# Kernel optimization log

Hardware: AMD Instinct MI355X
Metric: run time of the kernel (lower is better)

Reference implementation:

```python
import jax, jax.numpy as jnp
import numpy as np

B, N, M = 262144, 8, 4  # batch, state_dim, meas_dim
EPS = 1e-6


def _psd(key, b, d, scale=1.0):
    A = jax.random.normal(key, (b, d, d), dtype=jnp.float32)
    return (A @ jnp.swapaxes(A, 1, 2)) / d * scale + 0.1 * jnp.eye(d, dtype=jnp.float32)


def setup_inputs() -> dict:
    key = jax.random.key(0)
    ks = jax.random.split(key, 7)
    x_est = jax.random.normal(ks[0], (B, N, 1), dtype=jnp.float32)
    P_est = _psd(ks[1], B, N)
    F = jnp.eye(N, dtype=jnp.float32) + 0.1 * jax.random.normal(ks[2], (B, N, N), dtype=jnp.float32)
    Q = _psd(ks[3], B, N, scale=0.1)
    z = jax.random.normal(ks[4], (B, M, 1), dtype=jnp.float32)
    H = jax.random.normal(ks[5], (B, M, N), dtype=jnp.float32)
    R = _psd(ks[6], B, M, scale=0.5)
    return {"x_est": x_est, "P_est": P_est, "F": F, "Q": Q, "z": z, "H": H, "R": R}


def reference(x_est, P_est, F, Q, z, H, R):
    # Predict: x_pred = F x, P_pred = F P F^T + Q
    x_pred = F @ x_est                                     # [B,n,1]
    P_pred = F @ P_est @ jnp.swapaxes(F, 1, 2) + Q         # [B,n,n]
    # Update
    H_T = jnp.swapaxes(H, 1, 2)                            # [B,n,m]
    S = H @ P_pred @ H_T + R + EPS * jnp.eye(M, dtype=P_pred.dtype)  # [B,m,m]
    S_inv = jnp.linalg.inv(S)
    K = P_pred @ H_T @ S_inv                               # [B,n,m]
    y = z - H @ x_pred                                     # innovation [B,m,1]
    x_new = x_pred + K @ y
    IKH = jnp.eye(N, dtype=P_pred.dtype) - K @ H           # [B,n,n]
    P_new = IKH @ P_pred
    return x_new, P_new, K
```

## Files before the change

kernel.cpp:

```cpp
#include <hip/hip_runtime.h>


#define EPS 1e-6f
#define SYMIDX(r, c) ((r) * ((r) + 1) / 2 + (c))

typedef float v4f __attribute__((ext_vector_type(4)));

__device__ __forceinline__ void wave_lds_fence() {
    asm volatile("s_waitcnt lgkmcnt(0)" ::: "memory");
    __builtin_amdgcn_wave_barrier();
}

template <int W>
__device__ __forceinline__ void stage_load(float4 (&tmp)[W / 4], const float* __restrict__ src,
                                           int lane, int maxchunk) {
    const float4* s4 = reinterpret_cast<const float4*>(src);
#pragma unroll
    for (int i = 0; i < W / 4; ++i) {
        int c = i * 64 + lane;
        if (c >= maxchunk) c = maxchunk - 1;
        tmp[i] = s4[c];
    }
}

template <int W>
__device__ __forceinline__ void stage_write(const float4 (&tmp)[W / 4], float* buf, int lane) {
    constexpr int STR = W + 4;
#pragma unroll
    for (int i = 0; i < W / 4; ++i) {
        int c = i * 64 + lane;
        int bb = c / (W / 4);
        int e = c & (W / 4 - 1);
        *reinterpret_cast<float4*>(buf + bb * STR + e * 4) = tmp[i];
    }
}

__global__ __launch_bounds__(64) __attribute__((amdgpu_waves_per_eu(2, 4)))
void kf_kernel(const float* __restrict__ x_est,
               const float* __restrict__ P_est,
               const float* __restrict__ Fin,
               const float* __restrict__ Qin,
               const float* __restrict__ zin,
               const float* __restrict__ Hin,
               const float* __restrict__ Rin,
               float* __restrict__ out, int B) {
    const int lane = threadIdx.x;
    const int blockBase = blockIdx.x * 64;
    const int nb = (B - blockBase < 64) ? (B - blockBase) : 64;
    const int b = blockBase + lane;
    const size_t sb = (size_t)((b < B) ? b : (B - 1));
    const size_t wbase = (size_t)blockBase;

    __shared__ __align__(16) float buf[64 * 68];

    float4 zz = reinterpret_cast<const float4*>(zin)[sb];
    float4 xa = reinterpret_cast<const float4*>(x_est)[2 * sb];
    float4 xb = reinterpret_cast<const float4*>(x_est)[2 * sb + 1];

    float4 tF[16];
    stage_load<64>(tF, Fin + wbase * 64, lane, nb * 16);
    stage_write<64>(tF, buf, lane);

    float4 tP[16];
    stage_load<64>(tP, P_est + wbase * 64, lane, nb * 16);

    wave_lds_fence();
    float Fr[64];
    {
        const float* my = buf + lane * 68;
#pragma unroll
        for (int r = 0; r < 8; ++r) {
            float4 a = *reinterpret_cast<const float4*>(my + r * 8);
            float4 c4 = *reinterpret_cast<const float4*>(my + r * 8 + 4);
            Fr[r * 8 + 0] = a.x;  Fr[r * 8 + 1] = a.y;  Fr[r * 8 + 2] = a.z;  Fr[r * 8 + 3] = a.w;
            Fr[r * 8 + 4] = c4.x; Fr[r * 8 + 5] = c4.y; Fr[r * 8 + 6] = c4.z; Fr[r * 8 + 7] = c4.w;
        }
    }

    float xp[8];
    {
        float x[8] = {xa.x, xa.y, xa.z, xa.w, xb.x, xb.y, xb.z, xb.w};
#pragma unroll
        for (int i = 0; i < 8; ++i) {
            float s = 0.f;
#pragma unroll
            for (int j = 0; j < 8; ++j) s += Fr[i * 8 + j] * x[j];
            xp[i] = s;
        }
    }

    wave_lds_fence();
    stage_write<64>(tP, buf, lane);

    float4 tQ[16];
    stage_load<64>(tQ, Qin + wbase * 64, lane, nb * 16);

    wave_lds_fence();
    float Ps[36];
    {
        const float* my = buf + lane * 68;
#pragma unroll
        for (int r = 0; r < 8; ++r) {
            float4 a = *reinterpret_cast<const float4*>(my + r * 8);
            float row[8];
            row[0] = a.x; row[1] = a.y; row[2] = a.z; row[3] = a.w;
            row[4] = row[5] = row[6] = row[7] = 0.f;
            if (r >= 4) {
                float4 c4 = *reinterpret_cast<const float4*>(my + r * 8 + 4);
                row[4] = c4.x; row[5] = c4.y; row[6] = c4.z; row[7] = c4.w;
            }
#pragma unroll
            for (int j = 0; j <= r; ++j) Ps[SYMIDX(r, j)] = row[j];
        }
    }

    wave_lds_fence();
    stage_write<64>(tQ, buf, lane);

    float4 tH[8];
    stage_load<32>(tH, Hin + wbase * 32, lane, nb * 8);

    wave_lds_fence();
    float Pps[36];
    {
        const float* myq = buf + lane * 68;
#pragma unroll
        for (int i = 0; i < 8; ++i) {
            float Ti[8];
#pragma unroll
            for (int j = 0; j < 8; ++j) {
                float s = 0.f;
#pragma unroll
                for (int k = 0; k < 8; ++k) {
                    float pkj = (k >= j) ? Ps[SYMIDX(k, j)] : Ps[SYMIDX(j, k)];
                    s += Fr[i * 8 + k] * pkj;
                }
                Ti[j] = s;
            }
            float4 qa = *reinterpret_cast<const float4*>(myq + i * 8);
            float4 qb = qa;
            if (i >= 4) qb = *reinterpret_cast<const float4*>(myq + i * 8 + 4);
            float Qr[8] = {qa.x, qa.y, qa.z, qa.w, qb.x, qb.y, qb.z, qb.w};
#pragma unroll
            for (int j = 0; j <= i; ++j) {
                float s = Qr[j];
#pragma unroll
                for (int k = 0; k < 8; ++k) s += Ti[k] * Fr[j * 8 + k];
                Pps[SYMIDX(i, j)] = s;
            }
        }
    }

    wave_lds_fence();
    stage_write<32>(tH, buf, lane);

    float4 tR[4];
    stage_load<16>(tR, Rin + wbase * 16, lane, nb * 4);

    wave_lds_fence();
    float Hm[32];
    {
        const float* my = buf + lane * 36;
#pragma unroll
        for (int r = 0; r < 4; ++r) {
            float4 a = *reinterpret_cast<const float4*>(my + r * 8);
            float4 c4 = *reinterpret_cast<const float4*>(my + r * 8 + 4);
            Hm[r * 8 + 0] = a.x;  Hm[r * 8 + 1] = a.y;  Hm[r * 8 + 2] = a.z;  Hm[r * 8 + 3] = a.w;
            Hm[r * 8 + 4] = c4.x; Hm[r * 8 + 5] = c4.y; Hm[r * 8 + 6] = c4.z; Hm[r * 8 + 7] = c4.w;
        }
    }

    wave_lds_fence();
    stage_write<16>(tR, buf, lane);

    float HP[32];
#pragma unroll
    for (int i = 0; i < 4; ++i)
#pragma unroll
        for (int j = 0; j < 8; ++j) {
            float s = 0.f;
#pragma unroll
            for (int k = 0; k < 8; ++k) {
                float pkj = (k >= j) ? Pps[SYMIDX(k, j)] : Pps[SYMIDX(j, k)];
                s += Hm[i * 8 + k] * pkj;
            }
            HP[i * 8 + j] = s;
        }

    float y[4];
    {
        float zv[4] = {zz.x, zz.y, zz.z, zz.w};
#pragma unroll
        for (int i = 0; i < 4; ++i) {
            float s = zv[i];
#pragma unroll
            for (int k = 0; k < 8; ++k) s -= Hm[i * 8 + k] * xp[k];
            y[i] = s;
        }
    }

    wave_lds_fence();
    float S[16];
    {
        const float* my = buf + lane * 20;
#pragma unroll
        for (int i = 0; i < 4; ++i) {
            float4 r4 = *reinterpret_cast<const float4*>(my + i * 4);
            float Rr[4] = {r4.x, r4.y, r4.z, r4.w};
#pragma unroll
            for (int j = 0; j < 4; ++j) {
                float s = Rr[j];
#pragma unroll
                for (int k = 0; k < 8; ++k) s += HP[i * 8 + k] * Hm[j * 8 + k];
                if (i == j) s += EPS;
                S[i * 4 + j] = s;
            }
        }
    }

    float inv[16];
    inv[0]  =  S[5]*S[10]*S[15] - S[5]*S[11]*S[14] - S[9]*S[6]*S[15] + S[9]*S[7]*S[14] + S[13]*S[6]*S[11] - S[13]*S[7]*S[10];
    inv[4]  = -S[4]*S[10]*S[15] + S[4]*S[11]*S[14] + S[8]*S[6]*S[15] - S[8]*S[7]*S[14] - S[12]*S[6]*S[11] + S[12]*S[7]*S[10];
    inv[8]  =  S[4]*S[9]*S[15]  - S[4]*S[11]*S[13] - S[8]*S[5]*S[15] + S[8]*S[7]*S[13] + S[12]*S[5]*S[11] - S[12]*S[7]*S[9];
    inv[12] = -S[4]*S[9]*S[14]  + S[4]*S[10]*S[13] + S[8]*S[5]*S[14] - S[8]*S[6]*S[13] - S[12]*S[5]*S[10] + S[12]*S[6]*S[9];
    inv[1]  = -S[1]*S[10]*S[15] + S[1]*S[11]*S[14] + S[9]*S[2]*S[15] - S[9]*S[3]*S[14] - S[13]*S[2]*S[11] + S[13]*S[3]*S[10];
    inv[5]  =  S[0]*S[10]*S[15] - S[0]*S[11]*S[14] - S[8]*S[2]*S[15] + S[8]*S[3]*S[14] + S[12]*S[2]*S[11] - S[12]*S[3]*S[10];
    inv[9]  = -S[0]*S[9]*S[15]  + S[0]*S[11]*S[13] + S[8]*S[1]*S[15] - S[8]*S[3]*S[13] - S[12]*S[1]*S[11] + S[12]*S[3]*S[9];
    inv[13] =  S[0]*S[9]*S[14]  - S[0]*S[10]*S[13] - S[8]*S[1]*S[14] + S[8]*S[2]*S[13] + S[12]*S[1]*S[10] - S[12]*S[2]*S[9];
    inv[2]  =  S[1]*S[6]*S[15]  - S[1]*S[7]*S[14]  - S[5]*S[2]*S[15] + S[5]*S[3]*S[14] + S[13]*S[2]*S[7]  - S[13]*S[3]*S[6];
    inv[6]  = -S[0]*S[6]*S[15]  + S[0]*S[7]*S[14]  + S[4]*S[2]*S[15] - S[4]*S[3]*S[14] - S[12]*S[2]*S[7]  + S[12]*S[3]*S[6];
    inv[10] =  S[0]*S[5]*S[15]  - S[0]*S[7]*S[13]  - S[4]*S[1]*S[15] + S[4]*S[3]*S[13] + S[12]*S[1]*S[7]  - S[12]*S[3]*S[5];
    inv[14] = -S[0]*S[5]*S[14]  + S[0]*S[6]*S[13]  + S[4]*S[1]*S[14] - S[4]*S[2]*S[13] - S[12]*S[1]*S[6]  + S[12]*S[2]*S[5];
    inv[3]  = -S[1]*S[6]*S[11]  + S[1]*S[7]*S[10]  + S[5]*S[2]*S[11] - S[5]*S[3]*S[10] - S[9]*S[2]*S[7]   + S[9]*S[3]*S[6];
    inv[7]  =  S[0]*S[6]*S[11]  - S[0]*S[7]*S[10]  - S[4]*S[2]*S[11] + S[4]*S[3]*S[10] + S[8]*S[2]*S[7]   - S[8]*S[3]*S[6];
    inv[11] = -S[0]*S[5]*S[11]  + S[0]*S[7]*S[9]   + S[4]*S[1]*S[11] - S[4]*S[3]*S[9]  - S[8]*S[1]*S[7]   + S[8]*S[3]*S[5];
    inv[15] =  S[0]*S[5]*S[10]  - S[0]*S[6]*S[9]   - S[4]*S[1]*S[10] + S[4]*S[2]*S[9]  + S[8]*S[1]*S[6]   - S[8]*S[2]*S[5];
    float det = S[0]*inv[0] + S[1]*inv[4] + S[2]*inv[8] + S[3]*inv[12];
    float rdet = 1.0f / det;
#pragma unroll
    for (int i = 0; i < 16; ++i) inv[i] *= rdet;

    float K[32];
#pragma unroll
    for (int i = 0; i < 8; ++i)
#pragma unroll
        for (int j = 0; j < 4; ++j) {
            float s = 0.f;
#pragma unroll
            for (int k = 0; k < 4; ++k) s += HP[k * 8 + i] * inv[k * 4 + j];
            K[i * 4 + j] = s;
        }

    if (b < B) {
        float xn[8];
#pragma unroll
        for (int i = 0; i < 8; ++i) {
            float s = xp[i];
#pragma unroll
            for (int k = 0; k < 4; ++k) s += K[i * 4 + k] * y[k];
            xn[i] = s;
        }
        v4f v0 = {xn[0], xn[1], xn[2], xn[3]};
        v4f v1 = {xn[4], xn[5], xn[6], xn[7]};
        v4f* xo = reinterpret_cast<v4f*>(out + (size_t)b * 8);
        __builtin_nontemporal_store(v0, xo);
        __builtin_nontemporal_store(v1, xo + 1);
    }

    wave_lds_fence();
    {
        float* my = buf + lane * 68;
#pragma unroll
        for (int i = 0; i < 8; ++i) {
            float r[8];
#pragma unroll
            for (int j = 0; j < 8; ++j) {
                float pij = (i >= j) ? Pps[SYMIDX(i, j)] : Pps[SYMIDX(j, i)];
                float s = pij;
#pragma unroll
                for (int k = 0; k < 4; ++k) s -= K[i * 4 + k] * HP[k * 8 + j];
                r[j] = s;
            }
            *reinterpret_cast<float4*>(my + i * 8)     = make_float4(r[0], r[1], r[2], r[3]);
            *reinterpret_cast<float4*>(my + i * 8 + 4) = make_float4(r[4], r[5], r[6], r[7]);
        }
    }
    wave_lds_fence();
    {
        float* outP = out + (size_t)B * 8 + wbase * 64;
        const int maxc = nb * 16;
#pragma unroll
        for (int i = 0; i < 16; ++i) {
            int c = i * 64 + lane;
            if (c < maxc) {
                int bb = c >> 4, e = c & 15;
                v4f v = *reinterpret_cast<const v4f*>(buf + bb * 68 + e * 4);
                __builtin_nontemporal_store(v, reinterpret_cast<v4f*>(outP) + c);
            }
        }
    }

    wave_lds_fence();
    {
        float* my = buf + lane * 36;
#pragma unroll
        for (int i = 0; i < 8; ++i)
            *reinterpret_cast<float4*>(my + i * 4) =
                make_float4(K[4 * i + 0], K[4 * i + 1], K[4 * i + 2], K[4 * i + 3]);
    }
    wave_lds_fence();
    {
        float* outK = out + (size_t)B * 72 + wbase * 32;
        const int maxc = nb * 8;
#pragma unroll
        for (int i = 0; i < 8; ++i) {
            int c = i * 64 + lane;
            if (c < maxc) {
                int bb = c >> 3, e = c & 7;
                v4f v = *reinterpret_cast<const v4f*>(buf + bb * 36 + e * 4);
                __builtin_nontemporal_store(v, reinterpret_cast<v4f*>(outK) + c);
            }
        }
    }
}

extern "C" void kernel_launch(void* const* d_in, const int* in_sizes, int n_in,
                              void* d_out, int out_size, void* d_ws, size_t ws_size,
                              hipStream_t stream) {
    const float* x_est = (const float*)d_in[0];
    const float* P_est = (const float*)d_in[1];
    const float* F     = (const float*)d_in[2];
    const float* Q     = (const float*)d_in[3];
    const float* z     = (const float*)d_in[4];
    const float* H     = (const float*)d_in[5];
    const float* R     = (const float*)d_in[6];
    float* out = (float*)d_out;
    int B = in_sizes[0] / 8;
    int block = 64;
    int grid = (B + 63) / 64;
    kf_kernel<<<grid, block, 0, stream>>>(x_est, P_est, F, Q, z, H, R, out, B);
}
```

Baseline: 358.8 us.

## Persistent grid with async global-to-LDS prefetch of next group's F/P/Q

Converts the kernel to a persistent grid-stride loop over 64-batch groups, capped at 768 blocks. While the current group is computed, the next group's F, P and Q are prefetched straight into XOR-swizzled LDS using global_load_lds. H and R are now read per-thread directly from global memory. Outputs are written with plain per-thread strided stores instead of staging through LDS for coalescing. A hand-tuned vmcnt wait and the lower occupancy hint risk stalls, uncoalesced store traffic, or correctness issues if the counter count is wrong.

```diff
diff --git a/kernel.cpp b/kernel.cpp
--- a/kernel.cpp
+++ b/kernel.cpp
@@ -4,38 +4,27 @@
 #define EPS 1e-6f
 #define SYMIDX(r, c) ((r) * ((r) + 1) / 2 + (c))
 
-typedef float v4f __attribute__((ext_vector_type(4)));
-
-__device__ __forceinline__ void wave_lds_fence() {
-    asm volatile("s_waitcnt lgkmcnt(0)" ::: "memory");
-    __builtin_amdgcn_wave_barrier();
+__device__ __forceinline__ void gl_lds16(const float* g, float* l) {
+    __builtin_amdgcn_global_load_lds(
+        (const __attribute__((address_space(1))) void*)(uintptr_t)g,
+        (__attribute__((address_space(3))) void*)(unsigned)(uintptr_t)l,
+        16, 0, 0);
 }
 
-template <int W>
-__device__ __forceinline__ void stage_load(float4 (&tmp)[W / 4], const float* __restrict__ src,
-                                           int lane, int maxchunk) {
-    const float4* s4 = reinterpret_cast<const float4*>(src);
-#pragma unroll
-    for (int i = 0; i < W / 4; ++i) {
-        int c = i * 64 + lane;
-        if (c >= maxchunk) c = maxchunk - 1;
-        tmp[i] = s4[c];
+__device__ __forceinline__ void stage64(const float* __restrict__ src, int gstart,
+                                        float* ldsbase, int lane, int B) {
+#pragma unroll
+    for (int i = 0; i < 16; ++i) {
+        int b = i * 4 + (lane >> 4);
+        int e = lane & 15;
+        int gb = gstart + b;
+        if (gb > B - 1) gb = B - 1;
+        gl_lds16(src + (size_t)gb * 64 + (size_t)((e ^ (b & 7)) * 4),
+                 ldsbase + i * 256);
     }
 }
 
-template <int W>
-__device__ __forceinline__ void stage_write(const float4 (&tmp)[W / 4], float* buf, int lane) {
-    constexpr int STR = W + 4;
-#pragma unroll
-    for (int i = 0; i < W / 4; ++i) {
-        int c = i * 64 + lane;
-        int bb = c / (W / 4);
-        int e = c & (W / 4 - 1);
-        *reinterpret_cast<float4*>(buf + bb * STR + e * 4) = tmp[i];
-    }
-}
-
-__global__ __launch_bounds__(64) __attribute__((amdgpu_waves_per_eu(2, 4)))
+__global__ __launch_bounds__(64) __attribute__((amdgpu_waves_per_eu(1)))
 void kf_kernel(const float* __restrict__ x_est,
                const float* __restrict__ P_est,
                const float* __restrict__ Fin,
@@ -45,85 +34,115 @@
                const float* __restrict__ Rin,
                float* __restrict__ out, int B) {
     const int lane = threadIdx.x;
-    const int blockBase = blockIdx.x * 64;
-    const int nb = (B - blockBase < 64) ? (B - blockBase) : 64;
-    const int b = blockBase + lane;
-    const size_t sb = (size_t)((b < B) ? b : (B - 1));
-    const size_t wbase = (size_t)blockBase;
-
-    __shared__ __align__(16) float buf[64 * 68];
-
-    float4 zz = reinterpret_cast<const float4*>(zin)[sb];
-    float4 xa = reinterpret_cast<const float4*>(x_est)[2 * sb];
-    float4 xb = reinterpret_cast<const float4*>(x_est)[2 * sb + 1];
-
-    float4 tF[16];
-    stage_load<64>(tF, Fin + wbase * 64, lane, nb * 16);
-    stage_write<64>(tF, buf, lane);
-
-    float4 tP[16];
-    stage_load<64>(tP, P_est + wbase * 64, lane, nb * 16);
-
-    wave_lds_fence();
-    float Fr[64];
-    {
-        const float* my = buf + lane * 68;
+    const int ngroups = (B + 63) >> 6;
+    int g = blockIdx.x;
+    if (g >= ngroups) return;
+    const int stride = gridDim.x;
+
+    __shared__ __align__(16) float lds[12288];
+
+    stage64(Fin, g * 64, lds, lane, B);
+    stage64(P_est, g * 64, lds + 4096, lane, B);
+    stage64(Qin, g * 64, lds + 8192, lane, B);
+    int bc = g * 64 + lane;
+    if (bc > B - 1) bc = B - 1;
+    float4 zz = reinterpret_cast<const float4*>(zin)[bc];
+    float4 xa = reinterpret_cast<const float4*>(x_est)[2 * bc];
+    float4 xb = reinterpret_cast<const float4*>(x_est)[2 * bc + 1];
+    asm volatile("s_waitcnt vmcnt(0)" ::: "memory");
+
+    while (true) {
+        const int b0 = g * 64 + lane;
+        const bool full = (g * 64 + 64 <= B);
+        const int sw = lane & 7;
+        const float4* L4 = reinterpret_cast<const float4*>(lds);
+        const int gn = g + stride;
+        const int gnc = (gn < ngroups) ? gn : 0;
+
+        int b0c = (b0 > B - 1) ? B - 1 : b0;
+        float Hm[32];
+        {
+            const float4* H4 = reinterpret_cast<const float4*>(Hin + (size_t)b0c * 32);
+#pragma unroll
+            for (int i = 0; i < 8; ++i) {
+                float4 h = H4[i];
+                Hm[4 * i + 0] = h.x; Hm[4 * i + 1] = h.y; Hm[4 * i + 2] = h.z; Hm[4 * i + 3] = h.w;
+            }
+        }
+        const float4* Rp = reinterpret_cast<const float4*>(Rin + (size_t)b0c * 16);
+        float4 r0 = Rp[0], r1 = Rp[1], r2 = Rp[2], r3 = Rp[3];
+        int bcn = gnc * 64 + lane;
+        if (bcn > B - 1) bcn = B - 1;
+        float4 zzn = reinterpret_cast<const float4*>(zin)[bcn];
+        float4 xan = reinterpret_cast<const float4*>(x_est)[2 * bcn];
+        float4 xbn = reinterpret_cast<const float4*>(x_est)[2 * bcn + 1];
+
+        float Fr[64];
 #pragma unroll
         for (int r = 0; r < 8; ++r) {
-            float4 a = *reinterpret_cast<const float4*>(my + r * 8);
-            float4 c4 = *reinterpret_cast<const float4*>(my + r * 8 + 4);
-            Fr[r * 8 + 0] = a.x;  Fr[r * 8 + 1] = a.y;  Fr[r * 8 + 2] = a.z;  Fr[r * 8 + 3] = a.w;
-            Fr[r * 8 + 4] = c4.x; Fr[r * 8 + 5] = c4.y; Fr[r * 8 + 6] = c4.z; Fr[r * 8 + 7] = c4.w;
-        }
-    }
-
-    float xp[8];
-    {
-        float x[8] = {xa.x, xa.y, xa.z, xa.w, xb.x, xb.y, xb.z, xb.w};
-#pragma unroll
-        for (int i = 0; i < 8; ++i) {
-            float s = 0.f;
-#pragma unroll
-            for (int j = 0; j < 8; ++j) s += Fr[i * 8 + j] * x[j];
-            xp[i] = s;
-        }
-    }
-
-    wave_lds_fence();
-    stage_write<64>(tP, buf, lane);
-
-    float4 tQ[16];
-    stage_load<64>(tQ, Qin + wbase * 64, lane, nb * 16);
-
-    wave_lds_fence();
-    float Ps[36];
-    {
-        const float* my = buf + lane * 68;
+            float4 a = L4[lane * 16 + ((2 * r) ^ sw)];
+            float4 c = L4[lane * 16 + ((2 * r + 1) ^ sw)];
+            Fr[r * 8 + 0] = a.x; Fr[r * 8 + 1] = a.y; Fr[r * 8 + 2] = a.z; Fr[r * 8 + 3] = a.w;
+            Fr[r * 8 + 4] = c.x; Fr[r * 8 + 5] = c.y; Fr[r * 8 + 6] = c.z; Fr[r * 8 + 7] = c.w;
+        }
+        float Ps[36];
 #pragma unroll
         for (int r = 0; r < 8; ++r) {
-            float4 a = *reinterpret_cast<const float4*>(my + r * 8);
-            float row[8];
-            row[0] = a.x; row[1] = a.y; row[2] = a.z; row[3] = a.w;
-            row[4] = row[5] = row[6] = row[7] = 0.f;
-            if (r >= 4) {
-                float4 c4 = *reinterpret_cast<const float4*>(my + r * 8 + 4);
-                row[4] = c4.x; row[5] = c4.y; row[6] = c4.z; row[7] = c4.w;
-            }
-#pragma unroll
-            for (int j = 0; j <= r; ++j) Ps[SYMIDX(r, j)] = row[j];
-        }
-    }
-
-    wave_lds_fence();
-    stage_write<64>(tQ, buf, lane);
-
-    float4 tH[8];
-    stage_load<32>(tH, Hin + wbase * 32, lane, nb * 8);
-
-    wave_lds_fence();
-    float Pps[36];
-    {
-        const float* myq = buf + lane * 68;
+            float4 a = L4[1024 + lane * 16 + ((2 * r) ^ sw)];
+            float rw[4] = {a.x, a.y, a.z, a.w};
+            if (r < 4) {
+#pragma unroll
+                for (int j = 0; j < 4; ++j)
+                    if (j <= r) Ps[SYMIDX(r, j)] = rw[j];
+            } else {
+                float4 c = L4[1024 + lane * 16 + ((2 * r + 1) ^ sw)];
+                float rw2[4] = {c.x, c.y, c.z, c.w};
+#pragma unroll
+                for (int j = 0; j < 4; ++j) Ps[SYMIDX(r, j)] = rw[j];
+#pragma unroll
+                for (int j = 4; j < 8; ++j)
+                    if (j <= r) Ps[SYMIDX(r, j)] = rw2[j - 4];
+            }
+        }
+        float Qs[36];
+#pragma unroll
+        for (int r = 0; r < 8; ++r) {
+            float4 a = L4[2048 + lane * 16 + ((2 * r) ^ sw)];
+            float rw[4] = {a.x, a.y, a.z, a.w};
+            if (r < 4) {
+#pragma unroll
+                for (int j = 0; j < 4; ++j)
+                    if (j <= r) Qs[SYMIDX(r, j)] = rw[j];
+            } else {
+                float4 c = L4[2048 + lane * 16 + ((2 * r + 1) ^ sw)];
+                float rw2[4] = {c.x, c.y, c.z, c.w};
+#pragma unroll
+                for (int j = 0; j < 4; ++j) Qs[SYMIDX(r, j)] = rw[j];
+#pragma unroll
+                for (int j = 4; j < 8; ++j)
+                    if (j <= r) Qs[SYMIDX(r, j)] = rw2[j - 4];
+            }
+        }
+        asm volatile("s_waitcnt lgkmcnt(0)" ::: "memory");
+
+        stage64(Fin, gnc * 64, lds, lane, B);
+        stage64(P_est, gnc * 64, lds + 4096, lane, B);
+        stage64(Qin, gnc * 64, lds + 8192, lane, B);
+        asm volatile("" ::: "memory");
+
+        float xp[8];
+        {
+            float x[8] = {xa.x, xa.y, xa.z, xa.w, xb.x, xb.y, xb.z, xb.w};
+#pragma unroll
+            for (int i = 0; i < 8; ++i) {
+                float s = 0.f;
+#pragma unroll
+                for (int j = 0; j < 8; ++j) s += Fr[i * 8 + j] * x[j];
+                xp[i] = s;
+            }
+        }
+
+        float Pps[36];
 #pragma unroll
         for (int i = 0; i < 8; ++i) {
             float Ti[8];
@@ -137,190 +156,136 @@
                 }
                 Ti[j] = s;
             }
-            float4 qa = *reinterpret_cast<const float4*>(myq + i * 8);
-            float4 qb = qa;
-            if (i >= 4) qb = *reinterpret_cast<const float4*>(myq + i * 8 + 4);
-            float Qr[8] = {qa.x, qa.y, qa.z, qa.w, qb.x, qb.y, qb.z, qb.w};
 #pragma unroll
             for (int j = 0; j <= i; ++j) {
-                float s = Qr[j];
+                float s = Qs[SYMIDX(i, j)];
 #pragma unroll
                 for (int k = 0; k < 8; ++k) s += Ti[k] * Fr[j * 8 + k];
                 Pps[SYMIDX(i, j)] = s;
             }
         }
-    }
-
-    wave_lds_fence();
-    stage_write<32>(tH, buf, lane);
-
-    float4 tR[4];
-    stage_load<16>(tR, Rin + wbase * 16, lane, nb * 4);
-
-    wave_lds_fence();
-    float Hm[32];
-    {
-        const float* my = buf + lane * 36;
-#pragma unroll
-        for (int r = 0; r < 4; ++r) {
-            float4 a = *reinterpret_cast<const float4*>(my + r * 8);
-            float4 c4 = *reinterpret_cast<const float4*>(my + r * 8 + 4);
-            Hm[r * 8 + 0] = a.x;  Hm[r * 8 + 1] = a.y;  Hm[r * 8 + 2] = a.z;  Hm[r * 8 + 3] = a.w;
-            Hm[r * 8 + 4] = c4.x; Hm[r * 8 + 5] = c4.y; Hm[r * 8 + 6] = c4.z; Hm[r * 8 + 7] = c4.w;
-        }
-    }
-
-    wave_lds_fence();
-    stage_write<16>(tR, buf, lane);
-
-    float HP[32];
-#pragma unroll
-    for (int i = 0; i < 4; ++i)
-#pragma unroll
-        for (int j = 0; j < 8; ++j) {
-            float s = 0.f;
-#pragma unroll
-            for (int k = 0; k < 8; ++k) {
-                float pkj = (k >= j) ? Pps[SYMIDX(k, j)] : Pps[SYMIDX(j, k)];
-                s += Hm[i * 8 + k] * pkj;
-            }
-            HP[i * 8 + j] = s;
-        }
-
-    float y[4];
-    {
-        float zv[4] = {zz.x, zz.y, zz.z, zz.w};
-#pragma unroll
-        for (int i = 0; i < 4; ++i) {
-            float s = zv[i];
-#pragma unroll
-            for (int k = 0; k < 8; ++k) s -= Hm[i * 8 + k] * xp[k];
-            y[i] = s;
-        }
-    }
-
-    wave_lds_fence();
-    float S[16];
-    {
-        const float* my = buf + lane * 20;
-#pragma unroll
-        for (int i = 0; i < 4; ++i) {
-            float4 r4 = *reinterpret_cast<const float4*>(my + i * 4);
-            float Rr[4] = {r4.x, r4.y, r4.z, r4.w};
+
+        float HP[32];
+#pragma unroll
+        for (int i = 0; i < 4; ++i)
+#pragma unroll
+            for (int j = 0; j < 8; ++j) {
+                float s = 0.f;
+#pragma unroll
+                for (int k = 0; k < 8; ++k) {
+                    float pkj = (k >= j) ? Pps[SYMIDX(k, j)] : Pps[SYMIDX(j, k)];
+                    s += Hm[i * 8 + k] * pkj;
+                }
+                HP[i * 8 + j] = s;
+            }
+
+        float y[4];
+        {
+            float zv[4] = {zz.x, zz.y, zz.z, zz.w};
+#pragma unroll
+            for (int i = 0; i < 4; ++i) {
+                float s = zv[i];
+#pragma unroll
+                for (int k = 0; k < 8; ++k) s -= Hm[i * 8 + k] * xp[k];
+                y[i] = s;
+            }
+        }
+
+        float S[16];
+        {
+            float Rr[16] = {r0.x, r0.y, r0.z, r0.w, r1.x, r1.y, r1.z, r1.w,
+                            r2.x, r2.y, r2.z, r2.w, r3.x, r3.y, r3.z, r3.w};
+#pragma unroll
+            for (int i = 0; i < 4; ++i)
+#pragma unroll
+                for (int j = 0; j < 4; ++j) {
+                    float s = Rr[i * 4 + j];
+#pragma unroll
+                    for (int k = 0; k < 8; ++k) s += HP[i * 8 + k] * Hm[j * 8 + k];
+                    if (i == j) s += EPS;
+                    S[i * 4 + j] = s;
+                }
+        }
+
+        float inv[16];
+        inv[0]  =  S[5]*S[10]*S[15] - S[5]*S[11]*S[14] - S[9]*S[6]*S[15] + S[9]*S[7]*S[14] + S[13]*S[6]*S[11] - S[13]*S[7]*S[10];
+        inv[4]  = -S[4]*S[10]*S[15] + S[4]*S[11]*S[14] + S[8]*S[6]*S[15] - S[8]*S[7]*S[14] - S[12]*S[6]*S[11] + S[12]*S[7]*S[10];
+        inv[8]  =  S[4]*S[9]*S[15]  - S[4]*S[11]*S[13] - S[8]*S[5]*S[15] + S[8]*S[7]*S[13] + S[12]*S[5]*S[11] - S[12]*S[7]*S[9];
+        inv[12] = -S[4]*S[9]*S[14]  + S[4]*S[10]*S[13] + S[8]*S[5]*S[14] - S[8]*S[6]*S[13] - S[12]*S[5]*S[10] + S[12]*S[6]*S[9];
+        inv[1]  = -S[1]*S[10]*S[15] + S[1]*S[11]*S[14] + S[9]*S[2]*S[15] - S[9]*S[3]*S[14] - S[13]*S[2]*S[11] + S[13]*S[3]*S[10];
+        inv[5]  =  S[0]*S[10]*S[15] - S[0]*S[11]*S[14] - S[8]*S[2]*S[15] + S[8]*S[3]*S[14] + S[12]*S[2]*S[11] - S[12]*S[3]*S[10];
+        inv[9]  = -S[0]*S[9]*S[15]  + S[0]*S[11]*S[13] + S[8]*S[1]*S[15] - S[8]*S[3]*S[13] - S[12]*S[1]*S[11] + S[12]*S[3]*S[9];
+        inv[13] =  S[0]*S[9]*S[14]  - S[0]*S[10]*S[13] - S[8]*S[1]*S[14] + S[8]*S[2]*S[13] + S[12]*S[1]*S[10] - S[12]*S[2]*S[9];
+        inv[2]  =  S[1]*S[6]*S[15]  - S[1]*S[7]*S[14]  - S[5]*S[2]*S[15] + S[5]*S[3]*S[14] + S[13]*S[2]*S[7]  - S[13]*S[3]*S[6];
+        inv[6]  = -S[0]*S[6]*S[15]  + S[0]*S[7]*S[14]  + S[4]*S[2]*S[15] - S[4]*S[3]*S[14] - S[12]*S[2]*S[7]  + S[12]*S[3]*S[6];
+        inv[10] =  S[0]*S[5]*S[15]  - S[0]*S[7]*S[13]  - S[4]*S[1]*S[15] + S[4]*S[3]*S[13] + S[12]*S[1]*S[7]  - S[12]*S[3]*S[5];
+        inv[14] = -S[0]*S[5]*S[14]  + S[0]*S[6]*S[13]  + S[4]*S[1]*S[14] - S[4]*S[2]*S[13] - S[12]*S[1]*S[6]  + S[12]*S[2]*S[5];
+        inv[3]  = -S[1]*S[6]*S[11]  + S[1]*S[7]*S[10]  + S[5]*S[2]*S[11] - S[5]*S[3]*S[10] - S[9]*S[2]*S[7]   + S[9]*S[3]*S[6];
+        inv[7]  =  S[0]*S[6]*S[11]  - S[0]*S[7]*S[10]  - S[4]*S[2]*S[11] + S[4]*S[3]*S[10] + S[8]*S[2]*S[7]   - S[8]*S[3]*S[6];
+        inv[11] = -S[0]*S[5]*S[11]  + S[0]*S[7]*S[9]   + S[4]*S[1]*S[11] - S[4]*S[3]*S[9]  - S[8]*S[1]*S[7]   + S[8]*S[3]*S[5];
+        inv[15] =  S[0]*S[5]*S[10]  - S[0]*S[6]*S[9]   - S[4]*S[1]*S[10] + S[4]*S[2]*S[9]  + S[8]*S[1]*S[6]   - S[8]*S[2]*S[5];
+        float det = S[0]*inv[0] + S[1]*inv[4] + S[2]*inv[8] + S[3]*inv[12];
+        float rdet = 1.0f / det;
+#pragma unroll
+        for (int i = 0; i < 16; ++i) inv[i] *= rdet;
+
+        float K[32];
+#pragma unroll
+        for (int i = 0; i < 8; ++i)
 #pragma unroll
             for (int j = 0; j < 4; ++j) {
-                float s = Rr[j];
-#pragma unroll
-                for (int k = 0; k < 8; ++k) s += HP[i * 8 + k] * Hm[j * 8 + k];
-                if (i == j) s += EPS;
-                S[i * 4 + j] = s;
-            }
-        }
-    }
-
-    float inv[16];
-    inv[0]  =  S[5]*S[10]*S[15] - S[5]*S[11]*S[14] - S[9]*S[6]*S[15] + S[9]*S[7]*S[14] + S[13]*S[6]*S[11] - S[13]*S[7]*S[10];
-    inv[4]  = -S[4]*S[10]*S[15] + S[4]*S[11]*S[14] + S[8]*S[6]*S[15] - S[8]*S[7]*S[14] - S[12]*S[6]*S[11] + S[12]*S[7]*S[10];
-    inv[8]  =  S[4]*S[9]*S[15]  - S[4]*S[11]*S[13] - S[8]*S[5]*S[15] + S[8]*S[7]*S[13] + S[12]*S[5]*S[11] - S[12]*S[7]*S[9];
-    inv[12] = -S[4]*S[9]*S[14]  + S[4]*S[10]*S[13] + S[8]*S[5]*S[14] - S[8]*S[6]*S[13] - S[12]*S[5]*S[10] + S[12]*S[6]*S[9];
-    inv[1]  = -S[1]*S[10]*S[15] + S[1]*S[11]*S[14] + S[9]*S[2]*S[15] - S[9]*S[3]*S[14] - S[13]*S[2]*S[11] + S[13]*S[3]*S[10];
-    inv[5]  =  S[0]*S[10]*S[15] - S[0]*S[11]*S[14] - S[8]*S[2]*S[15] + S[8]*S[3]*S[14] + S[12]*S[2]*S[11] - S[12]*S[3]*S[10];
-    inv[9]  = -S[0]*S[9]*S[15]  + S[0]*S[11]*S[13] + S[8]*S[1]*S[15] - S[8]*S[3]*S[13] - S[12]*S[1]*S[11] + S[12]*S[3]*S[9];
-    inv[13] =  S[0]*S[9]*S[14]  - S[0]*S[10]*S[13] - S[8]*S[1]*S[14] + S[8]*S[2]*S[13] + S[12]*S[1]*S[10] - S[12]*S[2]*S[9];
-    inv[2]  =  S[1]*S[6]*S[15]  - S[1]*S[7]*S[14]  - S[5]*S[2]*S[15] + S[5]*S[3]*S[14] + S[13]*S[2]*S[7]  - S[13]*S[3]*S[6];
-    inv[6]  = -S[0]*S[6]*S[15]  + S[0]*S[7]*S[14]  + S[4]*S[2]*S[15] - S[4]*S[3]*S[14] - S[12]*S[2]*S[7]  + S[12]*S[3]*S[6];
-    inv[10] =  S[0]*S[5]*S[15]  - S[0]*S[7]*S[13]  - S[4]*S[1]*S[15] + S[4]*S[3]*S[13] + S[12]*S[1]*S[7]  - S[12]*S[3]*S[5];
-    inv[14] = -S[0]*S[5]*S[14]  + S[0]*S[6]*S[13]  + S[4]*S[1]*S[14] - S[4]*S[2]*S[13] - S[12]*S[1]*S[6]  + S[12]*S[2]*S[5];
-    inv[3]  = -S[1]*S[6]*S[11]  + S[1]*S[7]*S[10]  + S[5]*S[2]*S[11] - S[5]*S[3]*S[10] - S[9]*S[2]*S[7]   + S[9]*S[3]*S[6];
-    inv[7]  =  S[0]*S[6]*S[11]  - S[0]*S[7]*S[10]  - S[4]*S[2]*S[11] + S[4]*S[3]*S[10] + S[8]*S[2]*S[7]   - S[8]*S[3]*S[6];
-    inv[11] = -S[0]*S[5]*S[11]  + S[0]*S[7]*S[9]   + S[4]*S[1]*S[11] - S[4]*S[3]*S[9]  - S[8]*S[1]*S[7]   + S[8]*S[3]*S[5];
-    inv[15] =  S[0]*S[5]*S[10]  - S[0]*S[6]*S[9]   - S[4]*S[1]*S[10] + S[4]*S[2]*S[9]  + S[8]*S[1]*S[6]   - S[8]*S[2]*S[5];
-    float det = S[0]*inv[0] + S[1]*inv[4] + S[2]*inv[8] + S[3]*inv[12];
-    float rdet = 1.0f / det;
-#pragma unroll
-    for (int i = 0; i < 16; ++i) inv[i] *= rdet;
-
-    float K[32];
-#pragma unroll
-    for (int i = 0; i < 8; ++i)
-#pragma unroll
-        for (int j = 0; j < 4; ++j) {
-            float s = 0.f;
-#pragma unroll
-            for (int k = 0; k < 4; ++k) s += HP[k * 8 + i] * inv[k * 4 + j];
-            K[i * 4 + j] = s;
-        }
-
-    if (b < B) {
-        float xn[8];
-#pragma unroll
-        for (int i = 0; i < 8; ++i) {
-            float s = xp[i];
-#pragma unroll
-            for (int k = 0; k < 4; ++k) s += K[i * 4 + k] * y[k];
-            xn[i] = s;
-        }
-        v4f v0 = {xn[0], xn[1], xn[2], xn[3]};
-        v4f v1 = {xn[4], xn[5], xn[6], xn[7]};
-        v4f* xo = reinterpret_cast<v4f*>(out + (size_t)b * 8);
-        __builtin_nontemporal_store(v0, xo);
-        __builtin_nontemporal_store(v1, xo + 1);
-    }
-
-    wave_lds_fence();
-    {
-        float* my = buf + lane * 68;
-#pragma unroll
-        for (int i = 0; i < 8; ++i) {
-            float r[8];
-#pragma unroll
-            for (int j = 0; j < 8; ++j) {
-                float pij = (i >= j) ? Pps[SYMIDX(i, j)] : Pps[SYMIDX(j, i)];
-                float s = pij;
-#pragma unroll
-                for (int k = 0; k < 4; ++k) s -= K[i * 4 + k] * HP[k * 8 + j];
-                r[j] = s;
-            }
-            *reinterpret_cast<float4*>(my + i * 8)     = make_float4(r[0], r[1], r[2], r[3]);
-            *reinterpret_cast<float4*>(my + i * 8 + 4) = make_float4(r[4], r[5], r[6], r[7]);
-        }
-    }
-    wave_lds_fence();
-    {
-        float* outP = out + (size_t)B * 8 + wbase * 64;
-        const int maxc = nb * 16;
-#pragma unroll
-        for (int i = 0; i < 16; ++i) {
-            int c = i * 64 + lane;
-            if (c < maxc) {
-                int bb = c >> 4, e = c & 15;
-                v4f v = *reinterpret_cast<const v4f*>(buf + bb * 68 + e * 4);
-                __builtin_nontemporal_store(v, reinterpret_cast<v4f*>(outP) + c);
-            }
-        }
-    }
-
-    wave_lds_fence();
-    {
-        float* my = buf + lane * 36;
-#pragma unroll
-        for (int i = 0; i < 8; ++i)
-            *reinterpret_cast<float4*>(my + i * 4) =
-                make_float4(K[4 * i + 0], K[4 * i + 1], K[4 * i + 2], K[4 * i + 3]);
-    }
-    wave_lds_fence();
-    {
-        float* outK = out + (size_t)B * 72 + wbase * 32;
-        const int maxc = nb * 8;
-#pragma unroll
-        for (int i = 0; i < 8; ++i) {
-            int c = i * 64 + lane;
-            if (c < maxc) {
-                int bb = c >> 3, e = c & 7;
-                v4f v = *reinterpret_cast<const v4f*>(buf + bb * 36 + e * 4);
-                __builtin_nontemporal_store(v, reinterpret_cast<v4f*>(outK) + c);
-            }
-        }
+                float s = 0.f;
+#pragma unroll
+                for (int k = 0; k < 4; ++k) s += HP[k * 8 + i] * inv[k * 4 + j];
+                K[i * 4 + j] = s;
+            }
+
+        auto doStores = [&]() {
+            float4* xo = reinterpret_cast<float4*>(out + (size_t)b0 * 8);
+            float xn[8];
+#pragma unroll
+            for (int i = 0; i < 8; ++i) {
+                float s = xp[i];
+#pragma unroll
+                for (int k = 0; k < 4; ++k) s += K[i * 4 + k] * y[k];
+                xn[i] = s;
+            }
+            xo[0] = make_float4(xn[0], xn[1], xn[2], xn[3]);
+            xo[1] = make_float4(xn[4], xn[5], xn[6], xn[7]);
+
+            float4* po = reinterpret_cast<float4*>(out + (size_t)B * 8 + (size_t)b0 * 64);
+#pragma unroll
+            for (int i = 0; i < 8; ++i) {
+                float r[8];
+#pragma unroll
+                for (int j = 0; j < 8; ++j) {
+                    float pij = (i >= j) ? Pps[SYMIDX(i, j)] : Pps[SYMIDX(j, i)];
+                    float s = pij;
+#pragma unroll
+                    for (int k = 0; k < 4; ++k) s -= K[i * 4 + k] * HP[k * 8 + j];
+                    r[j] = s;
+                }
+                po[2 * i + 0] = make_float4(r[0], r[1], r[2], r[3]);
+                po[2 * i + 1] = make_float4(r[4], r[5], r[6], r[7]);
+            }
+
+            float4* ko = reinterpret_cast<float4*>(out + (size_t)B * 72 + (size_t)b0 * 32);
+#pragma unroll
+            for (int i = 0; i < 8; ++i)
+                ko[i] = make_float4(K[4 * i + 0], K[4 * i + 1], K[4 * i + 2], K[4 * i + 3]);
+        };
+
+        if (full) {
+            doStores();
+            asm volatile("s_waitcnt vmcnt(26)" ::: "memory");
+        } else {
+            if (b0 < B) doStores();
+            asm volatile("s_waitcnt vmcnt(0)" ::: "memory");
+        }
+
+        if (gn >= ngroups) break;
+        g = gn;
+        zz = zzn; xa = xan; xb = xbn;
     }
 }
 
@@ -336,7 +301,7 @@
     const float* R     = (const float*)d_in[6];
     float* out = (float*)d_out;
     int B = in_sizes[0] / 8;
-    int block = 64;
-    int grid = (B + 63) / 64;
-    kf_kernel<<<grid, block, 0, stream>>>(x_est, P_est, F, Q, z, H, R, out, B);
+    int ngroups = (B + 63) / 64;
+    int grid = ngroups < 768 ? ngroups : 768;
+    kf_kernel<<<grid, 64, 0, stream>>>(x_est, P_est, F, Q, z, H, R, out, B);
 }
```

Result: faster. 310.9 us (-13.4%).
